# Performance work log

Hardware: AMD Instinct MI355X
Metric: run time of the kernel (lower is better)

The kernel has to match this reference:

```python
import jax, jax.numpy as jnp
import numpy as np

BSZ, SEQ, NVARS = 4, 512, 7
DM, NH, DFF, EL, FACTOR, PRED = 512, 8, 2048, 2, 5, 96
DH = DM // NH


def layer_norm(x, g, b, eps=1e-5):
    mu = jnp.mean(x, -1, keepdims=True)
    var = jnp.mean((x - mu) ** 2, -1, keepdims=True)
    return (x - mu) / jnp.sqrt(var + eps) * g + b


def prob_attention(q, k, v, key, factor=FACTOR):
    # q,k,v: (B,H,L,D); Informer ProbSparse self-attention (non-causal)
    B, H, L, D = q.shape
    Lk = k.shape[2]
    U_part = min(int(factor * np.ceil(np.log(Lk))), Lk)  # sampled keys per query
    u = min(int(factor * np.ceil(np.log(L))), L)         # top queries kept
    idx = jax.random.randint(key, (L, U_part), 0, Lk)
    k_s = k[:, :, idx]                                   # (B,H,L,U,D) gathered keys
    qk_s = jnp.einsum('bhld,bhlud->bhlu', q, k_s)
    M = qk_s.max(-1) - qk_s.sum(-1) / Lk                 # sparsity measure (div by L_K, as in Informer)
    _, top = jax.lax.top_k(M, u)                         # (B,H,u) active query indices
    q_r = jnp.take_along_axis(q, top[..., None], axis=2)  # (B,H,u,D)
    scale = np.float32(1.0 / np.sqrt(D))
    scores = jnp.einsum('bhud,bhkd->bhuk', q_r, k) * scale
    attn = jax.nn.softmax(scores, axis=-1)
    upd = jnp.einsum('bhuk,bhkd->bhud', attn, v)
    # initial context = mean of V for every query; overwrite active queries
    ctx = jnp.broadcast_to(jnp.mean(v, axis=2, keepdims=True), (B, H, L, D))
    bi = jnp.arange(B)[:, None, None]
    hi = jnp.arange(H)[None, :, None]
    return ctx.at[bi, hi, top].set(upd)


def encoder_layer(x, p, key):
    Wq, bq, Wk, bk, Wv, bv, Wo, bo, W1, b1, W2, b2, g1, be1, g2, be2 = p
    B, L, _ = x.shape
    q = (x @ Wq.T + bq).reshape(B, L, NH, DH).transpose(0, 2, 1, 3)
    k = (x @ Wk.T + bk).reshape(B, L, NH, DH).transpose(0, 2, 1, 3)
    v = (x @ Wv.T + bv).reshape(B, L, NH, DH).transpose(0, 2, 1, 3)
    ctx = prob_attention(q, k, v, key)
    out = ctx.transpose(0, 2, 1, 3).reshape(B, L, DM) @ Wo.T + bo
    x = layer_norm(x + out, g1, be1)
    y = jax.nn.gelu(x @ W1.T + b1) @ W2.T + b2
    return layer_norm(x + y, g2, be2)


def _forward(x_enc, w_emb, b_emb, w_pos, Wq, bq, Wk, bk, Wv, bv, Wo, bo,
             W1, b1, W2, b2, g1, be1, g2, be2, gF, bF, Wh, bh):
    B, L, V = x_enc.shape
    emb = x_enc[..., None] * w_emb + b_emb               # (B,L,V,DM)  Linear(1,DM) per scalar
    h = emb.transpose(0, 2, 1, 3).reshape(B * V, L, DM) + w_pos
    base = jax.random.key(42)
    for l in range(EL):
        p = (Wq[l], bq[l], Wk[l], bk[l], Wv[l], bv[l], Wo[l], bo[l],
             W1[l], b1[l], W2[l], b2[l], g1[l], be1[l], g2[l], be2[l])
        h = encoder_layer(h, p, jax.random.fold_in(base, l))
    h = layer_norm(h, gF, bF)
    h = h.reshape(B, V, L * DM)                          # flatten head: nf = SEQ*DM
    out = h @ Wh.T + bh                                  # (B,V,PRED)
    return out.transpose(0, 2, 1)                        # (B,PRED,V)


def setup_inputs() -> dict:
    key = jax.random.key(0)
    ks = jax.random.split(key, 32)
    s = 0.02
    d = {
        'x_enc': jax.random.normal(ks[0], (BSZ, SEQ, NVARS), jnp.float32),
        'w_emb': jax.random.normal(ks[1], (DM,), jnp.float32) * s,
        'b_emb': jnp.zeros((DM,), jnp.float32),
        'w_pos': jax.random.normal(ks[2], (SEQ, DM), jnp.float32) * s,
        'Wq': jax.random.normal(ks[3], (EL, DM, DM), jnp.float32) * s,
        'bq': jnp.zeros((EL, DM), jnp.float32),
        'Wk': jax.random.normal(ks[4], (EL, DM, DM), jnp.float32) * s,
        'bk': jnp.zeros((EL, DM), jnp.float32),
        'Wv': jax.random.normal(ks[5], (EL, DM, DM), jnp.float32) * s,
        'bv': jnp.zeros((EL, DM), jnp.float32),
        'Wo': jax.random.normal(ks[6], (EL, DM, DM), jnp.float32) * s,
        'bo': jnp.zeros((EL, DM), jnp.float32),
        'W1': jax.random.normal(ks[7], (EL, DFF, DM), jnp.float32) * s,
        'b1': jnp.zeros((EL, DFF), jnp.float32),
        'W2': jax.random.normal(ks[8], (EL, DM, DFF), jnp.float32) * s,
        'b2': jnp.zeros((EL, DM), jnp.float32),
        'g1': jnp.ones((EL, DM), jnp.float32),
        'be1': jnp.zeros((EL, DM), jnp.float32),
        'g2': jnp.ones((EL, DM), jnp.float32),
        'be2': jnp.zeros((EL, DM), jnp.float32),
        'gF': jnp.ones((DM,), jnp.float32),
        'bF': jnp.zeros((DM,), jnp.float32),
        'Wh': jax.random.normal(ks[9], (PRED, SEQ * DM), jnp.float32) * 0.002,
        'bh': jnp.zeros((PRED,), jnp.float32),
    }
    return d


def reference(x_enc, w_emb, b_emb, w_pos, Wq, bq, Wk, bk, Wv, bv, Wo, bo,
              W1, b1, W2, b2, g1, be1, g2, be2, gF, bF, Wh, bh):
    return _forward(x_enc, w_emb, b_emb, w_pos, Wq, bq, Wk, bk, Wv, bv, Wo, bo,
                    W1, b1, W2, b2, g1, be1, g2, be2, gF, bF, Wh, bh)
```

## Files before the change

### kernel.cpp

```cpp
#include <hip/hip_runtime.h>
#include <math.h>

#define SEQL 512
#define DMOD 512
#define NHEAD 8
#define DHEAD 64
#define DFFN 2048
#define NBATCH 4
#define NVARS 7
#define NBV 28
#define NBH 224
#define NROWS 14336
#define NSAMP 35
#define NPRED 96
#define SBIG 7340032
#define QKS 1024

typedef short bf16x8 __attribute__((ext_vector_type(8)));
typedef float f32x4 __attribute__((ext_vector_type(4)));

__device__ inline unsigned short f2b(float f) {
  unsigned u = __builtin_bit_cast(unsigned, f);
  unsigned r = (u + 0x7FFFu + ((u >> 16) & 1u)) >> 16;
  return (unsigned short)r;
}
__device__ inline float b2f(unsigned short h) {
  return __builtin_bit_cast(float, (unsigned)h << 16);
}

__device__ inline void threefry2x32(unsigned k0, unsigned k1,
                                    unsigned x0, unsigned x1,
                                    unsigned &o0, unsigned &o1) {
  unsigned ks2 = k0 ^ k1 ^ 0x1BD11BDAu;
  unsigned ks[3] = {k0, k1, ks2};
  x0 += k0; x1 += k1;
  const unsigned rot[2][4] = {{13u,15u,26u,6u},{17u,29u,16u,24u}};
  #pragma unroll
  for (int i = 0; i < 5; ++i) {
    #pragma unroll
    for (int j = 0; j < 4; ++j) {
      unsigned r = rot[i & 1][j];
      x0 += x1;
      x1 = (x1 << r) | (x1 >> (32u - r));
      x1 ^= x0;
    }
    x0 += ks[(i + 1) % 3];
    x1 += ks[(i + 2) % 3] + (unsigned)(i + 1);
  }
  o0 = x0; o1 = x1;
}

__global__ void make_idx_kernel(int layer, int* idx) {
  int i = blockIdx.x * 256 + threadIdx.x;
  if (i >= SEQL * NSAMP) return;
  unsigned kl0, kl1, o0, o1;
  threefry2x32(0u, 42u, 0u, (unsigned)layer, kl0, kl1);
  threefry2x32(kl0, kl1, (unsigned)i, (unsigned)(SEQL * NSAMP + i), o0, o1);
  idx[i] = (int)(o1 & 511u);
}

__global__ void embed_kernel(const float* __restrict__ x_enc,
                             const float* __restrict__ w_emb,
                             const float* __restrict__ b_emb,
                             const float* __restrict__ w_pos,
                             float* __restrict__ h,
                             unsigned short* __restrict__ h_hi,
                             unsigned short* __restrict__ h_lo) {
  size_t i = (size_t)blockIdx.x * 256 + threadIdx.x;
  if (i >= (size_t)(SBIG / 4)) return;
  size_t e = i * 4;
  int dm = (int)(e & 511);
  int l  = (int)((e >> 9) & 511);
  int bv = (int)(e >> 18);
  int b = bv / NVARS, v = bv % NVARS;
  float xs = x_enc[((size_t)b * SEQL + l) * NVARS + v];
  float4 we = *(const float4*)(w_emb + dm);
  float4 bb = *(const float4*)(b_emb + dm);
  float4 wp = *(const float4*)(w_pos + (size_t)l * DMOD + dm);
  float4 val;
  val.x = xs * we.x + bb.x + wp.x;
  val.y = xs * we.y + bb.y + wp.y;
  val.z = xs * we.z + bb.z + wp.z;
  val.w = xs * we.w + bb.w + wp.w;
  *(float4*)(h + e) = val;
  ushort4 hi4, lo4;
  hi4.x = f2b(val.x); lo4.x = f2b(val.x - b2f(hi4.x));
  hi4.y = f2b(val.y); lo4.y = f2b(val.y - b2f(hi4.y));
  hi4.z = f2b(val.z); lo4.z = f2b(val.z - b2f(hi4.z));
  hi4.w = f2b(val.w); lo4.w = f2b(val.w - b2f(hi4.w));
  *(ushort4*)(h_hi + e) = hi4;
  *(ushort4*)(h_lo + e) = lo4;
}

__global__ void prep_weights(const float* __restrict__ Wq, const float* __restrict__ Wk,
                             const float* __restrict__ Wv, const float* __restrict__ Wo,
                             const float* __restrict__ W1, const float* __restrict__ W2,
                             unsigned short* __restrict__ Wqk_hi, unsigned short* __restrict__ Wqk_lo,
                             unsigned short* __restrict__ Wv_b, unsigned short* __restrict__ Wo_b,
                             unsigned short* __restrict__ W1_b, unsigned short* __restrict__ W2_b) {
  const int Q4 = 65536;
  int g = blockIdx.x * 256 + threadIdx.x;
  if (g < 2 * Q4) {
    const float* src = g < Q4 ? Wq : Wk;
    unsigned short* hi = Wqk_hi + (g < Q4 ? 0 : DMOD * DMOD);
    unsigned short* lo = Wqk_lo + (g < Q4 ? 0 : DMOD * DMOD);
    int off = (g < Q4 ? g : g - Q4) * 4;
    float4 v = *(const float4*)(src + off);
    ushort4 h4, l4;
    h4.x = f2b(v.x); l4.x = f2b(v.x - b2f(h4.x));
    h4.y = f2b(v.y); l4.y = f2b(v.y - b2f(h4.y));
    h4.z = f2b(v.z); l4.z = f2b(v.z - b2f(h4.z));
    h4.w = f2b(v.w); l4.w = f2b(v.w - b2f(h4.w));
    *(ushort4*)(hi + off) = h4;
    *(ushort4*)(lo + off) = l4;
    return;
  }
  const float* src;
  unsigned short* dst;
  int off;
  if (g < 3 * Q4)      { src = Wv; dst = Wv_b; off = (g - 2 * Q4) * 4; }
  else if (g < 4 * Q4) { src = Wo; dst = Wo_b; off = (g - 3 * Q4) * 4; }
  else if (g < 4 * Q4 + 262144) { src = W1; dst = W1_b; off = (g - 4 * Q4) * 4; }
  else                 { src = W2; dst = W2_b; off = (g - 4 * Q4 - 262144) * 4; }
  float4 v = *(const float4*)(src + off);
  ushort4 o;
  o.x = f2b(v.x); o.y = f2b(v.y); o.z = f2b(v.z); o.w = f2b(v.w);
  *(ushort4*)(dst + off) = o;
}

__global__ __launch_bounds__(256) void gemm_mfma3(const unsigned short* __restrict__ Ah,
                                                  const unsigned short* __restrict__ Al,
                                                  const unsigned short* __restrict__ Bh,
                                                  const unsigned short* __restrict__ Bl,
                                                  const float* __restrict__ bq,
                                                  const float* __restrict__ bk,
                                                  float* __restrict__ C,
                                                  int M, int N, int K, int ldc) {
  __shared__ __align__(16) unsigned short AsH[128 * 64];
  __shared__ __align__(16) unsigned short AsL[128 * 64];
  __shared__ __align__(16) unsigned short BsH[128 * 64];
  __shared__ __align__(16) unsigned short BsL[128 * 64];
  int nwg = gridDim.x * gridDim.y;
  int flat = blockIdx.y * gridDim.x + blockIdx.x;
  int swz = (flat & 7) * (nwg >> 3) + (flat >> 3);
  int bxs = swz % gridDim.x, bys = swz / gridDim.x;
  int bm = bys * 128, bn = bxs * 128;
  int tid = threadIdx.x;
  int wave = tid >> 6, lane = tid & 63;
  int wr = wave >> 1, wc = wave & 1;
  int r16 = lane & 15, kq = lane >> 4;

  f32x4 acc[4][4];
  #pragma unroll
  for (int i = 0; i < 4; ++i)
    #pragma unroll
    for (int j = 0; j < 4; ++j) acc[i][j] = (f32x4){0.f, 0.f, 0.f, 0.f};

  for (int kt = 0; kt < K; kt += 64) {
    __syncthreads();
    #pragma unroll
    for (int i = 0; i < 4; ++i) {
      int c = i * 256 + tid;
      int row = c >> 3, kb = c & 7;
      size_t offA = (size_t)(bm + row) * K + kt + kb * 8;
      size_t offB = (size_t)(bn + row) * K + kt + kb * 8;
      uint4 vah = *(const uint4*)(Ah + offA);
      uint4 val = *(const uint4*)(Al + offA);
      uint4 vbh = *(const uint4*)(Bh + offB);
      uint4 vbl = *(const uint4*)(Bl + offB);
      int sw = ((row << 7) | (kb << 4)) ^ ((row & 7) << 4);
      *(uint4*)((char*)AsH + sw) = vah;
      *(uint4*)((char*)AsL + sw) = val;
      *(uint4*)((char*)BsH + sw) = vbh;
      *(uint4*)((char*)BsL + sw) = vbl;
    }
    __syncthreads();
    #pragma unroll
    for (int ks = 0; ks < 2; ++ks) {
      bf16x8 ah[4], al[4], bh[4], bl[4];
      #pragma unroll
      for (int mi = 0; mi < 4; ++mi) {
        int row = wr * 64 + mi * 16 + r16;
        int addr = ((row << 7) | (ks << 6) | (kq << 4)) ^ ((row & 7) << 4);
        ah[mi] = *(const bf16x8*)((const char*)AsH + addr);
        al[mi] = *(const bf16x8*)((const char*)AsL + addr);
      }
      #pragma unroll
      for (int ni = 0; ni < 4; ++ni) {
        int row = wc * 64 + ni * 16 + r16;
        int addr = ((row << 7) | (ks << 6) | (kq << 4)) ^ ((row & 7) << 4);
        bh[ni] = *(const bf16x8*)((const char*)BsH + addr);
        bl[ni] = *(const bf16x8*)((const char*)BsL + addr);
      }
      #pragma unroll
      for (int mi = 0; mi < 4; ++mi)
        #pragma unroll
        for (int ni = 0; ni < 4; ++ni) {
          acc[mi][ni] = __builtin_amdgcn_mfma_f32_16x16x32_bf16(ah[mi], bh[ni], acc[mi][ni], 0, 0, 0);
          acc[mi][ni] = __builtin_amdgcn_mfma_f32_16x16x32_bf16(ah[mi], bl[ni], acc[mi][ni], 0, 0, 0);
          acc[mi][ni] = __builtin_amdgcn_mfma_f32_16x16x32_bf16(al[mi], bh[ni], acc[mi][ni], 0, 0, 0);
        }
    }
  }
  int crow0 = bm + wr * 64 + (lane >> 4) * 4;
  int ccol0 = bn + wc * 64 + (lane & 15);
  #pragma unroll
  for (int mi = 0; mi < 4; ++mi) {
    #pragma unroll
    for (int ni = 0; ni < 4; ++ni) {
      int col = ccol0 + ni * 16;
      float bvv = col < 512 ? bq[col] : bk[col - 512];
      #pragma unroll
      for (int r = 0; r < 4; ++r) {
        int row = crow0 + mi * 16 + r;
        C[(size_t)row * ldc + col] = acc[mi][ni][r] + bvv;
      }
    }
  }
}

template<int ACT, int OUTBF>
__global__ __launch_bounds__(256) void gemm_mfma(const unsigned short* __restrict__ A,
                                                 const unsigned short* __restrict__ W,
                                                 const float* __restrict__ bias,
                                                 float* __restrict__ Cf,
                                                 unsigned short* __restrict__ Cb,
                                                 int M, int N, int K) {
  __shared__ __align__(16) unsigned short As[128 * 64];
  __shared__ __align__(16) unsigned short Bs[128 * 64];
  int nwg = gridDim.x * gridDim.y;
  int flat = blockIdx.y * gridDim.x + blockIdx.x;
  int swz = (flat & 7) * (nwg >> 3) + (flat >> 3);
  int bxs = swz % gridDim.x, bys = swz / gridDim.x;
  int bm = bys * 128, bn = bxs * 128;
  int tid = threadIdx.x;
  int wave = tid >> 6, lane = tid & 63;
  int wr = wave >> 1, wc = wave & 1;
  int r16 = lane & 15, kq = lane >> 4;

  f32x4 acc[4][4];
  #pragma unroll
  for (int i = 0; i < 4; ++i)
    #pragma unroll
    for (int j = 0; j < 4; ++j) acc[i][j] = (f32x4){0.f, 0.f, 0.f, 0.f};

  for (int kt = 0; kt < K; kt += 64) {
    __syncthreads();
    #pragma unroll
    for (int i = 0; i < 4; ++i) {
      int c = i * 256 + tid;
      int row = c >> 3, kb = c & 7;
      uint4 va = *(const uint4*)(A + (size_t)(bm + row) * K + kt + kb * 8);
      uint4 vb = *(const uint4*)(W + (size_t)(bn + row) * K + kt + kb * 8);
      int sw = ((row << 7) | (kb << 4)) ^ ((row & 7) << 4);
      *(uint4*)((char*)As + sw) = va;
      *(uint4*)((char*)Bs + sw) = vb;
    }
    __syncthreads();
    #pragma unroll
    for (int ks = 0; ks < 2; ++ks) {
      bf16x8 afr[4], bfr[4];
      #pragma unroll
      for (int mi = 0; mi < 4; ++mi) {
        int row = wr * 64 + mi * 16 + r16;
        int addr = ((row << 7) | (ks << 6) | (kq << 4)) ^ ((row & 7) << 4);
        afr[mi] = *(const bf16x8*)((const char*)As + addr);
      }
      #pragma unroll
      for (int ni = 0; ni < 4; ++ni) {
        int row = wc * 64 + ni * 16 + r16;
        int addr = ((row << 7) | (ks << 6) | (kq << 4)) ^ ((row & 7) << 4);
        bfr[ni] = *(const bf16x8*)((const char*)Bs + addr);
      }
      #pragma unroll
      for (int mi = 0; mi < 4; ++mi)
        #pragma unroll
        for (int ni = 0; ni < 4; ++ni)
          acc[mi][ni] = __builtin_amdgcn_mfma_f32_16x16x32_bf16(afr[mi], bfr[ni], acc[mi][ni], 0, 0, 0);
    }
  }
  int crow0 = bm + wr * 64 + (lane >> 4) * 4;
  int ccol0 = bn + wc * 64 + (lane & 15);
  #pragma unroll
  for (int mi = 0; mi < 4; ++mi) {
    #pragma unroll
    for (int ni = 0; ni < 4; ++ni) {
      int col = ccol0 + ni * 16;
      float bvv = bias[col];
      #pragma unroll
      for (int r = 0; r < 4; ++r) {
        int row = crow0 + mi * 16 + r;
        float v = acc[mi][ni][r] + bvv;
        if (ACT) {
          float x = v;
          float t = tanhf(0.7978845608028654f * (x + 0.044715f * x * x * x));
          v = 0.5f * x * (1.0f + t);
        }
        if (OUTBF) Cb[(size_t)row * N + col] = f2b(v);
        else       Cf[(size_t)row * N + col] = v;
      }
    }
  }
}

__global__ __launch_bounds__(512) void m2_kernel(const float* __restrict__ QK,
                                                 const int* __restrict__ idx,
                                                 float* __restrict__ Mout) {
  int bh = blockIdx.x;
  int bv = bh >> 3, head = bh & 7;
  int tid = threadIdx.x;
  __shared__ float Ks[512 * 65];
  const float* base = QK + (size_t)bv * (SEQL * QKS);
  for (int c = tid; c < 512 * 16; c += 512) {
    int l = c >> 4, d4 = (c & 15) * 4;
    float4 v = *(const float4*)(base + (size_t)l * QKS + 512 + head * 64 + d4);
    Ks[l * 65 + d4 + 0] = v.x;
    Ks[l * 65 + d4 + 1] = v.y;
    Ks[l * 65 + d4 + 2] = v.z;
    Ks[l * 65 + d4 + 3] = v.w;
  }
  float q[64];
  const float* qp = base + (size_t)tid * QKS + head * 64;
  #pragma unroll
  for (int d4 = 0; d4 < 64; d4 += 4) {
    float4 qv = *(const float4*)(qp + d4);
    q[d4 + 0] = qv.x; q[d4 + 1] = qv.y; q[d4 + 2] = qv.z; q[d4 + 3] = qv.w;
  }
  __syncthreads();
  const int* ip = idx + tid * NSAMP;
  float mx = -INFINITY, sm = 0.f;
  for (int u = 0; u < NSAMP; ++u) {
    int kidx = ip[u];
    const float* kr = Ks + kidx * 65;
    float s = 0.f;
    #pragma unroll
    for (int d = 0; d < 64; ++d) s += q[d] * kr[d];
    mx = fmaxf(mx, s);
    sm += s;
  }
  Mout[(size_t)bh * SEQL + tid] = mx - sm * (1.0f / 512.0f);
}

__global__ __launch_bounds__(256) void topk_kernel(const float* __restrict__ Mv,
                                                   int* __restrict__ top) {
  int bh = blockIdx.x;
  int tid = threadIdx.x;
  __shared__ float vals[512];
  __shared__ float rv[256];
  __shared__ int ri[256];
  vals[tid]       = Mv[(size_t)bh * SEQL + tid];
  vals[tid + 256] = Mv[(size_t)bh * SEQL + tid + 256];
  __syncthreads();
  for (int t = 0; t < NSAMP; ++t) {
    float v0 = vals[tid], v1 = vals[tid + 256];
    float bvv; int bii;
    if (v0 >= v1) { bvv = v0; bii = tid; } else { bvv = v1; bii = tid + 256; }
    rv[tid] = bvv; ri[tid] = bii;
    __syncthreads();
    for (int s = 128; s > 0; s >>= 1) {
      if (tid < s) {
        float ov = rv[tid + s]; int oi = ri[tid + s];
        if (ov > rv[tid] || (ov == rv[tid] && oi < ri[tid])) { rv[tid] = ov; ri[tid] = oi; }
      }
      __syncthreads();
    }
    if (tid == 0) { top[bh * NSAMP + t] = ri[0]; vals[ri[0]] = -INFINITY; }
    __syncthreads();
  }
}

__global__ __launch_bounds__(64) void vmean_kernel(const unsigned short* __restrict__ Vb,
                                                   float* __restrict__ vmean) {
  int bh = blockIdx.x;
  int bv = bh >> 3, head = bh & 7;
  int d = threadIdx.x;
  const unsigned short* vb = Vb + (size_t)bv * (SEQL * DMOD) + head * 64 + d;
  float s = 0.f;
  for (int l = 0; l < SEQL; ++l) s += b2f(vb[(size_t)l * DMOD]);
  vmean[bh * DHEAD + d] = s * (1.0f / 512.0f);
}

__global__ void ctx_fill_kernel(const float* __restrict__ vmean,
                                unsigned short* __restrict__ ctxb) {
  size_t i = (size_t)blockIdx.x * 256 + threadIdx.x;
  if (i >= (size_t)(SBIG / 4)) return;
  size_t e = i * 4;
  int dm = (int)(e & 511);
  int bv = (int)(e >> 18);
  float4 vm = *(const float4*)(vmean + bv * DMOD + dm);
  ushort4 o;
  o.x = f2b(vm.x); o.y = f2b(vm.y); o.z = f2b(vm.z); o.w = f2b(vm.w);
  *(ushort4*)(ctxb + e) = o;
}

__global__ __launch_bounds__(256) void attn2_kernel(const float* __restrict__ QK,
                                                    const unsigned short* __restrict__ Vb,
                                                    const int* __restrict__ top,
                                                    unsigned short* __restrict__ ctxb) {
  __shared__ __align__(16) unsigned short KV[512 * 64];
  __shared__ __align__(16) unsigned short P[48 * 512];
  __shared__ __align__(16) unsigned short Qs[48 * 64];
  __shared__ int topi[NSAMP];
  int bh = blockIdx.x;
  int bv = bh >> 3, head = bh & 7;
  int tid = threadIdx.x;
  int wv = tid >> 6, lane = tid & 63;
  int r16 = lane & 15, kq = lane >> 4;
  const float* base = QK + (size_t)bv * (SEQL * QKS);
  const unsigned short* vbase = Vb + (size_t)bv * (SEQL * DMOD) + head * 64;

  if (tid < NSAMP) topi[tid] = top[bh * NSAMP + tid];
  __syncthreads();

  for (int c = tid; c < NSAMP * 16; c += 256) {
    int u = c >> 4, dq = c & 15;
    float4 q4 = *(const float4*)(base + (size_t)topi[u] * QKS + head * 64 + dq * 4);
    ushort4 o;
    o.x = f2b(q4.x * 0.125f); o.y = f2b(q4.y * 0.125f);
    o.z = f2b(q4.z * 0.125f); o.w = f2b(q4.w * 0.125f);
    int byte = ((u << 7) | (dq << 3)) ^ ((u & 7) << 4);
    *(ushort4*)((char*)Qs + byte) = o;
  }
  for (int c = tid; c < 512 * 16; c += 256) {
    int l = c >> 4, dq = c & 15;
    float4 k4 = *(const float4*)(base + (size_t)l * QKS + 512 + head * 64 + dq * 4);
    ushort4 o;
    o.x = f2b(k4.x); o.y = f2b(k4.y); o.z = f2b(k4.z); o.w = f2b(k4.w);
    int byte = ((l << 7) | (dq << 3)) ^ ((l & 7) << 4);
    *(ushort4*)((char*)KV + byte) = o;
  }
  __syncthreads();

  {
    f32x4 acc[3][8];
    #pragma unroll
    for (int m = 0; m < 3; ++m)
      #pragma unroll
      for (int j = 0; j < 8; ++j) acc[m][j] = (f32x4){0.f, 0.f, 0.f, 0.f};
    bf16x8 afr[3][2];
    #pragma unroll
    for (int m = 0; m < 3; ++m)
      #pragma unroll
      for (int ks = 0; ks < 2; ++ks) {
        int row = m * 16 + r16;
        int addr = ((row << 7) | (ks << 6) | (kq << 4)) ^ ((row & 7) << 4);
        afr[m][ks] = *(const bf16x8*)((const char*)Qs + addr);
      }
    #pragma unroll
    for (int j = 0; j < 8; ++j) {
      int nrow = (wv * 8 + j) * 16 + r16;
      #pragma unroll
      for (int ks = 0; ks < 2; ++ks) {
        int addr = ((nrow << 7) | (ks << 6) | (kq << 4)) ^ ((nrow & 7) << 4);
        bf16x8 bfr = *(const bf16x8*)((const char*)KV + addr);
        #pragma unroll
        for (int m = 0; m < 3; ++m)
          acc[m][j] = __builtin_amdgcn_mfma_f32_16x16x32_bf16(afr[m][ks], bfr, acc[m][j], 0, 0, 0);
      }
    }
    #pragma unroll
    for (int m = 0; m < 3; ++m)
      #pragma unroll
      for (int j = 0; j < 8; ++j) {
        int l = (wv * 8 + j) * 16 + r16;
        #pragma unroll
        for (int r = 0; r < 4; ++r) {
          int u = m * 16 + kq * 4 + r;
          int byte = ((u << 10) | (l << 1)) ^ ((u & 7) << 4);
          *(unsigned short*)((char*)P + byte) = f2b(acc[m][j][r]);
        }
      }
  }
  __syncthreads();

  for (int c = tid; c < 512 * 8; c += 256) {
    int l = c >> 3, dq = c & 7;
    bf16x8 v8 = *(const bf16x8*)(vbase + (size_t)l * DMOD + dq * 8);
    #pragma unroll
    for (int j = 0; j < 8; ++j) {
      int d = dq * 8 + j;
      int byte = ((d << 10) | (l << 1)) ^ ((d & 7) << 4);
      *(unsigned short*)((char*)KV + byte) = (unsigned short)v8[j];
    }
  }
  for (int u = wv; u < NSAMP; u += 4) {
    int byte = ((u << 10) | (lane << 4)) ^ ((u & 7) << 4);
    bf16x8 sv = *(const bf16x8*)((const char*)P + byte);
    float s[8];
    #pragma unroll
    for (int j = 0; j < 8; ++j) s[j] = b2f((unsigned short)sv[j]);
    float mx = s[0];
    #pragma unroll
    for (int j = 1; j < 8; ++j) mx = fmaxf(mx, s[j]);
    #pragma unroll
    for (int off = 32; off > 0; off >>= 1) mx = fmaxf(mx, __shfl_xor(mx, off));
    float e[8], sm = 0.f;
    #pragma unroll
    for (int j = 0; j < 8; ++j) { e[j] = __expf(s[j] - mx); sm += e[j]; }
    #pragma unroll
    for (int off = 32; off > 0; off >>= 1) sm += __shfl_xor(sm, off);
    float inv = 1.0f / sm;
    bf16x8 pv;
    #pragma unroll
    for (int j = 0; j < 8; ++j) pv[j] = (short)f2b(e[j] * inv);
    *(bf16x8*)((char*)P + byte) = pv;
  }
  __syncthreads();

  {
    f32x4 acc2[3];
    #pragma unroll
    for (int m = 0; m < 3; ++m) acc2[m] = (f32x4){0.f, 0.f, 0.f, 0.f};
    for (int kst = 0; kst < 16; ++kst) {
      int vrow = wv * 16 + r16;
      int baddr = ((vrow << 10) | (kst << 6) | (kq << 4)) ^ ((vrow & 7) << 4);
      bf16x8 bfr = *(const bf16x8*)((const char*)KV + baddr);
      #pragma unroll
      for (int m = 0; m < 3; ++m) {
        int prow = m * 16 + r16;
        int aaddr = ((prow << 10) | (kst << 6) | (kq << 4)) ^ ((prow & 7) << 4);
        bf16x8 afr2 = *(const bf16x8*)((const char*)P + aaddr);
        acc2[m] = __builtin_amdgcn_mfma_f32_16x16x32_bf16(afr2, bfr, acc2[m], 0, 0, 0);
      }
    }
    int d = wv * 16 + r16;
    #pragma unroll
    for (int m = 0; m < 3; ++m)
      #pragma unroll
      for (int r = 0; r < 4; ++r) {
        int u = m * 16 + kq * 4 + r;
        if (u < NSAMP) {
          size_t off = (size_t)bv * (SEQL * DMOD) + (size_t)topi[u] * DMOD + head * 64 + d;
          ctxb[off] = f2b(acc2[m][r]);
        }
      }
  }
}

template<int BMODE, int OUT>
__global__ __launch_bounds__(256) void add_ln(const float* __restrict__ a,
                                              const unsigned short* __restrict__ b,
                                              const float* __restrict__ g,
                                              const float* __restrict__ be,
                                              float* __restrict__ out,
                                              unsigned short* __restrict__ outb,
                                              unsigned short* __restrict__ outh,
                                              unsigned short* __restrict__ outl) {
  int row = blockIdx.x * 2 + (threadIdx.x >> 7);
  int t = threadIdx.x & 127;
  int wave = threadIdx.x >> 6;
  int lane = threadIdx.x & 63;
  size_t base = (size_t)row * DMOD + t * 4;
  float4 x = *(const float4*)(a + base);
  if (BMODE == 2) {
    ushort4 r4 = *(const ushort4*)(b + base);
    x.x += b2f(r4.x); x.y += b2f(r4.y); x.z += b2f(r4.z); x.w += b2f(r4.w);
  }
  float s1 = x.x + x.y + x.z + x.w;
  float s2 = x.x * x.x + x.y * x.y + x.z * x.z + x.w * x.w;
  #pragma unroll
  for (int off = 32; off > 0; off >>= 1) {
    s1 += __shfl_xor(s1, off);
    s2 += __shfl_xor(s2, off);
  }
  __shared__ float sh[8];
  if (lane == 0) { sh[wave * 2] = s1; sh[wave * 2 + 1] = s2; }
  __syncthreads();
  int mate = wave ^ 1;
  s1 += sh[mate * 2];
  s2 += sh[mate * 2 + 1];
  float mu = s1 * (1.0f / 512.0f);
  float var = s2 * (1.0f / 512.0f) - mu * mu;
  float rstd = rsqrtf(var + 1e-5f);
  float4 gg = *(const float4*)(g + t * 4);
  float4 bb = *(const float4*)(be + t * 4);
  float4 o;
  o.x = (x.x - mu) * rstd * gg.x + bb.x;
  o.y = (x.y - mu) * rstd * gg.y + bb.y;
  o.z = (x.z - mu) * rstd * gg.z + bb.z;
  o.w = (x.w - mu) * rstd * gg.w + bb.w;
  *(float4*)(out + base) = o;
  if (OUT == 1) {
    ushort4 ob;
    ob.x = f2b(o.x); ob.y = f2b(o.y); ob.z = f2b(o.z); ob.w = f2b(o.w);
    *(ushort4*)(outb + base) = ob;
  }
  if (OUT == 2) {
    ushort4 hi4, lo4;
    hi4.x = f2b(o.x); lo4.x = f2b(o.x - b2f(hi4.x));
    hi4.y = f2b(o.y); lo4.y = f2b(o.y - b2f(hi4.y));
    hi4.z = f2b(o.z); lo4.z = f2b(o.z - b2f(hi4.z));
    hi4.w = f2b(o.w); lo4.w = f2b(o.w - b2f(hi4.w));
    *(ushort4*)(outh + base) = hi4;
    *(ushort4*)(outl + base) = lo4;
  }
}

__global__ __launch_bounds__(256) void head_partial_mfma(const unsigned short* __restrict__ hbf,
                                                         const float* __restrict__ Wh,
                                                         float* __restrict__ partial) {
  __shared__ __align__(16) unsigned short Hs[32 * 512];
  __shared__ __align__(16) unsigned short Ws[96 * 512];
  int blk = blockIdx.x;
  int k0 = blk * 512;
  int tid = threadIdx.x;
  int wv = tid >> 6, lane = tid & 63;
  int r16 = lane & 15, kq = lane >> 4;

  for (int c = tid; c < 32 * 64; c += 256) {
    int row = c >> 6, col8 = c & 63;
    int src = row < 28 ? row : 0;
    bf16x8 v = *(const bf16x8*)(hbf + (size_t)src * 262144 + k0 + col8 * 8);
    int byte = ((row << 10) | (col8 << 4)) ^ ((row & 7) << 4);
    *(bf16x8*)((char*)Hs + byte) = v;
  }
  for (int c = tid; c < 96 * 64; c += 256) {
    int row = c >> 6, col8 = c & 63;
    const float* src = Wh + (size_t)row * 262144 + k0 + col8 * 8;
    float4 va = *(const float4*)(src);
    float4 vb = *(const float4*)(src + 4);
    bf16x8 o8;
    o8[0] = (short)f2b(va.x); o8[1] = (short)f2b(va.y);
    o8[2] = (short)f2b(va.z); o8[3] = (short)f2b(va.w);
    o8[4] = (short)f2b(vb.x); o8[5] = (short)f2b(vb.y);
    o8[6] = (short)f2b(vb.z); o8[7] = (short)f2b(vb.w);
    int byte = ((row << 10) | (col8 << 4)) ^ ((row & 7) << 4);
    *(bf16x8*)((char*)Ws + byte) = o8;
  }
  __syncthreads();

  f32x4 acc[2][6];
  #pragma unroll
  for (int mt = 0; mt < 2; ++mt)
    #pragma unroll
    for (int nt = 0; nt < 6; ++nt) acc[mt][nt] = (f32x4){0.f, 0.f, 0.f, 0.f};

  #pragma unroll
  for (int kk = 0; kk < 4; ++kk) {
    int kfrag = wv * 4 + kk;
    bf16x8 afr[2];
    #pragma unroll
    for (int mt = 0; mt < 2; ++mt) {
      int row = mt * 16 + r16;
      int byte = ((row << 10) | (kfrag << 6) | (kq << 4)) ^ ((row & 7) << 4);
      afr[mt] = *(const bf16x8*)((const char*)Hs + byte);
    }
    #pragma unroll
    for (int nt = 0; nt < 6; ++nt) {
      int row = nt * 16 + r16;
      int byte = ((row << 10) | (kfrag << 6) | (kq << 4)) ^ ((row & 7) << 4);
      bf16x8 bfr = *(const bf16x8*)((const char*)Ws + byte);
      #pragma unroll
      for (int mt = 0; mt < 2; ++mt)
        acc[mt][nt] = __builtin_amdgcn_mfma_f32_16x16x32_bf16(afr[mt], bfr, acc[mt][nt], 0, 0, 0);
    }
  }
  size_t prow = (size_t)(blk * 4 + wv) * 2688;
  #pragma unroll
  for (int mt = 0; mt < 2; ++mt)
    #pragma unroll
    for (int nt = 0; nt < 6; ++nt)
      #pragma unroll
      for (int r = 0; r < 4; ++r) {
        int m = mt * 16 + kq * 4 + r;
        int n = nt * 16 + r16;
        if (m < 28) partial[prow + m * 96 + n] = acc[mt][nt][r];
      }
}

__global__ __launch_bounds__(256) void head_reduce(const float* __restrict__ partial,
                                                   const float* __restrict__ bh_,
                                                   float* __restrict__ out) {
  int o = blockIdx.x;
  int tid = threadIdx.x;
  float s = 0.f;
  for (int b = tid; b < 2048; b += 256) s += partial[(size_t)b * 2688 + o];
  __shared__ float red[256];
  red[tid] = s;
  __syncthreads();
  for (int st = 128; st > 0; st >>= 1) {
    if (tid < st) red[tid] += red[tid + st];
    __syncthreads();
  }
  if (tid == 0) {
    int m = o / 96, p = o % 96;
    int b = m / NVARS, v = m % NVARS;
    out[(size_t)b * (NPRED * NVARS) + (size_t)p * NVARS + v] = red[0] + bh_[p];
  }
}

extern "C" void kernel_launch(void* const* d_in, const int* in_sizes, int n_in,
                              void* d_out, int out_size, void* d_ws, size_t ws_size,
                              hipStream_t stream) {
  const float* x_enc = (const float*)d_in[0];
  const float* w_emb = (const float*)d_in[1];
  const float* b_emb = (const float*)d_in[2];
  const float* w_pos = (const float*)d_in[3];
  const float* Wq = (const float*)d_in[4];
  const float* bq = (const float*)d_in[5];
  const float* Wk = (const float*)d_in[6];
  const float* bk = (const float*)d_in[7];
  const float* Wv = (const float*)d_in[8];
  const float* bv_ = (const float*)d_in[9];
  const float* Wo = (const float*)d_in[10];
  const float* bo = (const float*)d_in[11];
  const float* W1 = (const float*)d_in[12];
  const float* b1 = (const float*)d_in[13];
  const float* W2 = (const float*)d_in[14];
  const float* b2 = (const float*)d_in[15];
  const float* g1 = (const float*)d_in[16];
  const float* be1 = (const float*)d_in[17];
  const float* g2 = (const float*)d_in[18];
  const float* be2 = (const float*)d_in[19];
  const float* gF = (const float*)d_in[20];
  const float* bF = (const float*)d_in[21];
  const float* Wh = (const float*)d_in[22];
  const float* bh_ = (const float*)d_in[23];
  float* out = (float*)d_out;

  const size_t S = (size_t)SBIG;
  const size_t SB = S * 4;
  char* ws = (char*)d_ws;
  float* h    = (float*)(ws);
  float* QKb  = (float*)(ws + SB);
  unsigned short* Vb   = (unsigned short*)(ws + 3 * SB);
  unsigned short* Ob_b = (unsigned short*)(ws + 3 * SB + SB / 2);
  unsigned short* Wqk_hi = (unsigned short*)(ws + 4 * SB);
  unsigned short* Wqk_lo = (unsigned short*)(ws + 4 * SB + 0x100000);
  unsigned short* Wv_b = (unsigned short*)(ws + 4 * SB + 0x200000);
  unsigned short* Wo_b = (unsigned short*)(ws + 4 * SB + 0x280000);
  unsigned short* W1_b = (unsigned short*)(ws + 4 * SB + 0x300000);
  unsigned short* W2_b = (unsigned short*)(ws + 4 * SB + 0x500000);
  unsigned short* h_hi = (unsigned short*)(ws + 5 * SB);
  unsigned short* h_lo = (unsigned short*)(ws + 5 * SB + SB / 2);
  unsigned short* CTXb = h_hi;
  unsigned short* h_bf = h_lo;
  unsigned short* FFNb = (unsigned short*)QKb;
  float* partial = QKb;
  int*   idx = (int*)(ws + 6 * SB);
  float* Mv  = (float*)(ws + 6 * SB + 0x20000);
  int*   top = (int*)(ws + 6 * SB + 0xA0000);
  float* vmean = (float*)(ws + 6 * SB + 0xB0000);
  if (ws_size < 6 * SB + 0xC0000) return;

  dim3 b256(256);
  int gVec = (int)(S / 4 / 256);

  embed_kernel<<<gVec, b256, 0, stream>>>(x_enc, w_emb, b_emb, w_pos, h, h_hi, h_lo);

  for (int l = 0; l < 2; ++l) {
    const float* Wql = Wq + (size_t)l * DMOD * DMOD;
    const float* Wkl = Wk + (size_t)l * DMOD * DMOD;
    const float* Wvl = Wv + (size_t)l * DMOD * DMOD;
    const float* Wol = Wo + (size_t)l * DMOD * DMOD;
    const float* W1l = W1 + (size_t)l * DFFN * DMOD;
    const float* W2l = W2 + (size_t)l * DMOD * DFFN;

    prep_weights<<<3072, b256, 0, stream>>>(Wql, Wkl, Wvl, Wol, W1l, W2l,
                                            Wqk_hi, Wqk_lo, Wv_b, Wo_b, W1_b, W2_b);

    dim3 gqk(QKS / 128, NROWS / 128);
    gemm_mfma3<<<gqk, b256, 0, stream>>>(h_hi, h_lo, Wqk_hi, Wqk_lo,
                                         bq + l * DMOD, bk + l * DMOD,
                                         QKb, NROWS, QKS, DMOD, QKS);
    dim3 gv(DMOD / 128, NROWS / 128);
    gemm_mfma<0, 1><<<gv, b256, 0, stream>>>(h_hi, Wv_b, bv_ + l * DMOD,
                                             (float*)0, Vb, NROWS, DMOD, DMOD);

    make_idx_kernel<<<(SEQL * NSAMP + 255) / 256, b256, 0, stream>>>(l, idx);
    m2_kernel<<<NBH, dim3(512), 0, stream>>>(QKb, idx, Mv);
    topk_kernel<<<NBH, b256, 0, stream>>>(Mv, top);
    vmean_kernel<<<NBH, dim3(64), 0, stream>>>(Vb, vmean);
    ctx_fill_kernel<<<gVec, b256, 0, stream>>>(vmean, CTXb);
    attn2_kernel<<<NBH, b256, 0, stream>>>(QKb, Vb, top, CTXb);

    dim3 go(DMOD / 128, NROWS / 128);
    gemm_mfma<0, 1><<<go, b256, 0, stream>>>(CTXb, Wo_b, bo + l * DMOD,
                                             (float*)0, Ob_b, NROWS, DMOD, DMOD);
    add_ln<2, 1><<<NROWS / 2, b256, 0, stream>>>(h, Ob_b, g1 + l * DMOD, be1 + l * DMOD,
                                                 h, h_bf, (unsigned short*)0, (unsigned short*)0);

    dim3 gf1(DFFN / 128, NROWS / 128);
    gemm_mfma<1, 1><<<gf1, b256, 0, stream>>>(h_bf, W1_b, b1 + l * DFFN,
                                              (float*)0, FFNb, NROWS, DFFN, DMOD);
    dim3 gf2(DMOD / 128, NROWS / 128);
    gemm_mfma<0, 1><<<gf2, b256, 0, stream>>>(FFNb, W2_b, b2 + l * DMOD,
                                              (float*)0, Ob_b, NROWS, DMOD, DFFN);
    if (l == 0) {
      add_ln<2, 2><<<NROWS / 2, b256, 0, stream>>>(h, Ob_b, g2 + l * DMOD, be2 + l * DMOD,
                                                   h, (unsigned short*)0, h_hi, h_lo);
    } else {
      add_ln<2, 0><<<NROWS / 2, b256, 0, stream>>>(h, Ob_b, g2 + l * DMOD, be2 + l * DMOD,
                                                   h, (unsigned short*)0, (unsigned short*)0, (unsigned short*)0);
    }
  }

  add_ln<0, 1><<<NROWS / 2, b256, 0, stream>>>(h, (const unsigned short*)0, gF, bF,
                                               h, h_bf, (unsigned short*)0, (unsigned short*)0);
  head_partial_mfma<<<512, b256, 0, stream>>>(h_bf, Wh, partial);
  head_reduce<<<NBV * NPRED, b256, 0, stream>>>(partial, bh_, out);
}
```

Baseline: 822.3 us.

## Use sigmoid-form GELU, XOR-swizzled float4 K tile, and vectorized V-mean

The FFN epilogue computes tanh-GELU as x*sigmoid(2y) with a fast __expf instead of tanhf. This is mathematically equivalent, though it has slightly different rounding. The m2 kernel stores K in shared memory without padding, using an XOR swizzle so that both the writes and the per-sample dot products use float4 accesses instead of scalar loads. The V-mean kernel now uses one 256-thread block per batch-variable and reads two bf16 values per thread in coalesced 32-bit loads, replacing the 64-thread per-head blocks that read single shorts.

```diff
diff --git a/kernel.cpp b/kernel.cpp
--- a/kernel.cpp
+++ b/kernel.cpp
@@ -293,8 +293,8 @@
         float v = acc[mi][ni][r] + bvv;
         if (ACT) {
           float x = v;
-          float t = tanhf(0.7978845608028654f * (x + 0.044715f * x * x * x));
-          v = 0.5f * x * (1.0f + t);
+          float y2 = 1.5957691216057308f * (x + 0.044715f * x * x * x);
+          v = x / (1.0f + __expf(-y2));
         }
         if (OUTBF) Cb[(size_t)row * N + col] = f2b(v);
         else       Cf[(size_t)row * N + col] = v;
@@ -309,15 +309,12 @@
   int bh = blockIdx.x;
   int bv = bh >> 3, head = bh & 7;
   int tid = threadIdx.x;
-  __shared__ float Ks[512 * 65];
+  __shared__ float Ks[512 * 64];
   const float* base = QK + (size_t)bv * (SEQL * QKS);
   for (int c = tid; c < 512 * 16; c += 512) {
-    int l = c >> 4, d4 = (c & 15) * 4;
-    float4 v = *(const float4*)(base + (size_t)l * QKS + 512 + head * 64 + d4);
-    Ks[l * 65 + d4 + 0] = v.x;
-    Ks[l * 65 + d4 + 1] = v.y;
-    Ks[l * 65 + d4 + 2] = v.z;
-    Ks[l * 65 + d4 + 3] = v.w;
+    int l = c >> 4, db = c & 15;
+    float4 v = *(const float4*)(base + (size_t)l * QKS + 512 + head * 64 + db * 4);
+    *(float4*)(Ks + l * 64 + ((db ^ (l & 15)) << 2)) = v;
   }
   float q[64];
   const float* qp = base + (size_t)tid * QKS + head * 64;
@@ -331,10 +328,15 @@
   float mx = -INFINITY, sm = 0.f;
   for (int u = 0; u < NSAMP; ++u) {
     int kidx = ip[u];
-    const float* kr = Ks + kidx * 65;
+    const float* kr = Ks + kidx * 64;
+    int x = kidx & 15;
     float s = 0.f;
     #pragma unroll
-    for (int d = 0; d < 64; ++d) s += q[d] * kr[d];
+    for (int db = 0; db < 16; ++db) {
+      float4 kv = *(const float4*)(kr + ((db ^ x) << 2));
+      s += q[db * 4 + 0] * kv.x + q[db * 4 + 1] * kv.y
+         + q[db * 4 + 2] * kv.z + q[db * 4 + 3] * kv.w;
+    }
     mx = fmaxf(mx, s);
     sm += s;
   }
@@ -369,15 +371,20 @@
   }
 }
 
-__global__ __launch_bounds__(64) void vmean_kernel(const unsigned short* __restrict__ Vb,
-                                                   float* __restrict__ vmean) {
-  int bh = blockIdx.x;
-  int bv = bh >> 3, head = bh & 7;
-  int d = threadIdx.x;
-  const unsigned short* vb = Vb + (size_t)bv * (SEQL * DMOD) + head * 64 + d;
-  float s = 0.f;
-  for (int l = 0; l < SEQL; ++l) s += b2f(vb[(size_t)l * DMOD]);
-  vmean[bh * DHEAD + d] = s * (1.0f / 512.0f);
+__global__ __launch_bounds__(256) void vmean_kernel(const unsigned short* __restrict__ Vb,
+                                                    float* __restrict__ vmean) {
+  int bv = blockIdx.x;
+  int t = threadIdx.x;
+  const unsigned short* vb = Vb + (size_t)bv * (SEQL * DMOD) + t * 2;
+  float s0 = 0.f, s1 = 0.f;
+  #pragma unroll 4
+  for (int l = 0; l < SEQL; ++l) {
+    unsigned u = *(const unsigned*)(vb + (size_t)l * DMOD);
+    s0 += b2f((unsigned short)(u & 0xffffu));
+    s1 += b2f((unsigned short)(u >> 16));
+  }
+  vmean[bv * DMOD + t * 2]     = s0 * (1.0f / 512.0f);
+  vmean[bv * DMOD + t * 2 + 1] = s1 * (1.0f / 512.0f);
 }
 
 __global__ void ctx_fill_kernel(const float* __restrict__ vmean,
@@ -770,7 +777,7 @@
     make_idx_kernel<<<(SEQL * NSAMP + 255) / 256, b256, 0, stream>>>(l, idx);
     m2_kernel<<<NBH, dim3(512), 0, stream>>>(QKb, idx, Mv);
     topk_kernel<<<NBH, b256, 0, stream>>>(Mv, top);
-    vmean_kernel<<<NBH, dim3(64), 0, stream>>>(Vb, vmean);
+    vmean_kernel<<<NBV, b256, 0, stream>>>(Vb, vmean);
     ctx_fill_kernel<<<gVec, b256, 0, stream>>>(vmean, CTXb);
     attn2_kernel<<<NBH, b256, 0, stream>>>(QKb, Vb, top, CTXb);
 
```

Result: no change. 806.9 us (-1.9%).
